# Kernel optimization log

Measured on AMD Instinct MI355X. Metric: run time of the kernel, lower is better.

## Reference

```python
import jax, jax.numpy as jnp
import numpy as np

N = 10000        # nodes
E = 320000       # edges
IN = 256         # input_dim
D = 64           # output_dim per head
H = 4            # num_heads
ED = 32          # edge_dim
T = 8            # num_etypes
SLOPE = 0.2      # leaky relu negative slope


def setup_inputs() -> dict:
    key = jax.random.key(0)
    ks = jax.random.split(key, 12)
    s = 0.05
    feat = jax.random.normal(ks[0], (N, IN), jnp.float32)
    edge_weight = jax.random.uniform(ks[1], (E,), jnp.float32)
    row = jax.random.randint(ks[2], (E,), 0, N, jnp.int32)
    col = jax.random.randint(ks[3], (E,), 0, N, jnp.int32)
    etype_idxs = jax.random.randint(ks[4], (E,), 0, T, jnp.int32)
    W = jax.random.normal(ks[5], (IN, D * H), jnp.float32) * s
    edge_emb_table = jax.random.normal(ks[6], (T, ED), jnp.float32) * s
    W_r = jax.random.normal(ks[7], (T, ED, ED * H), jnp.float32) * s
    a_l = jax.random.normal(ks[8], (H, D), jnp.float32) * s
    a_r = jax.random.normal(ks[9], (H, D), jnp.float32) * s
    a_e = jax.random.normal(ks[10], (H, ED), jnp.float32) * s
    W_res = jax.random.normal(ks[11], (IN, D * H), jnp.float32) * s
    b_res = jnp.zeros((D * H,), jnp.float32)
    return dict(feat=feat, edge_weight=edge_weight, row=row, col=col,
                etype_idxs=etype_idxs, W=W, edge_emb_table=edge_emb_table,
                W_r=W_r, a_l=a_l, a_r=a_r, a_e=a_e, W_res=W_res, b_res=b_res)


def reference(feat, edge_weight, row, col, etype_idxs, W, edge_emb_table,
              W_r, a_l, a_r, a_e, W_res, b_res):
    # node projection: [N, H, D]
    emb = jnp.nan_to_num(feat @ W).reshape(N, H, D)
    # typed linear on edge-type embeddings: only T distinct outputs, gather per edge
    type_out = jnp.einsum('ti,tio->to', edge_emb_table, W_r).reshape(T, H, ED)
    edge_e = type_out[etype_idxs]                      # [E, H, ED]
    # attention logits
    hl = jnp.einsum('nhd,hd->nh', emb, a_l)            # [N, H]
    hr = jnp.einsum('nhd,hd->nh', emb, a_r)            # [N, H]
    he = jnp.einsum('ehd,hd->eh', edge_e, a_e)         # [E, H]
    att = jax.nn.sigmoid(jax.nn.leaky_relu(hl[row] + hr[col] + he, SLOPE))
    att = att * edge_weight[:, None]                   # [E, H]
    # u_mul_e + sum scatter: src=row, dst=col
    msg = emb[row] * att[:, :, None]                   # [E, H, D]
    agg = jax.ops.segment_sum(msg, col, num_segments=N)  # [N, H, D]
    # original permutes to [N, D, H] before flattening
    out = jnp.transpose(agg, (0, 2, 1)).reshape(N, D * H)
    out = out + feat @ W_res + b_res                   # residual
    return jax.nn.elu(out)
```

## Files before the change

### kernel.cpp

```cpp
#include <hip/hip_runtime.h>
#include <hip/hip_bf16.h>
#include <math.h>

#define N_NODES 10000
#define MPAD 10112
#define N_EDGES 320000
#define IN_DIM 256
#define NH 4
#define EDIM 32
#define NT 8
#define SLOPE 0.2f
#define CAP 96

#define WTW (512 * 256)
#define GB (MPAD / 64)
#define EBT 512
#define EB ((N_EDGES + EBT - 1) / EBT)

typedef __attribute__((ext_vector_type(8))) short short8b;
typedef __attribute__((ext_vector_type(4))) float f32x4;

__device__ __forceinline__ float bf2f(ushort u) {
  return __uint_as_float(((unsigned)u) << 16);
}
__device__ __forceinline__ ushort f2bf(float f) {
  __hip_bfloat16 h = __float2bfloat16(f);
  return *(ushort*)&h;
}
__device__ __forceinline__ unsigned pk2(float a, float b) {
  return (unsigned)f2bf(a) | ((unsigned)f2bf(b) << 16);
}

__global__ void prep_kernel(const float* __restrict__ W,
                            const float* __restrict__ W_res,
                            const float* __restrict__ table,
                            const float* __restrict__ W_r,
                            const float* __restrict__ a_e,
                            ushort* __restrict__ Wtb,
                            float* __restrict__ he_type,
                            int* __restrict__ cnt) {
  int i = blockIdx.x * 256 + threadIdx.x;
  if (i < WTW) {
    int c = i >> 8, k = i & 255;
    float v = (c < 256) ? W[k * 256 + ((c & 3) * 64 + (c >> 2))]
                        : W_res[k * 256 + (c - 256)];
    Wtb[c * 256 + k] = f2bf(v);
  } else if (i < WTW + 1024) {
    int t2 = i - WTW;
    int t = t2 >> 7, h = (t2 >> 5) & 3, d = t2 & 31;
    float acc = 0.f;
    for (int q = 0; q < EDIM; ++q)
      acc += table[t * EDIM + q] * W_r[(t * EDIM + q) * (EDIM * NH) + h * EDIM + d];
    acc *= a_e[h * EDIM + d];
#pragma unroll
    for (int o = 16; o; o >>= 1) acc += __shfl_xor(acc, o, 32);
    if (d == 0) he_type[t * NH + h] = acc;
  } else {
    int z = i - WTW - 1024;
    if (z <= N_NODES) cnt[z] = 0;
  }
}

__global__ __launch_bounds__(512) void gemm_bucket_kernel(
    const float* __restrict__ feat, const ushort* __restrict__ Wtb,
    const float* __restrict__ b_res,
    const float* __restrict__ a_l, const float* __restrict__ a_r,
    ushort* __restrict__ emb_t, ushort* __restrict__ resb,
    float* __restrict__ hl, float* __restrict__ hr,
    const int* __restrict__ row, const int* __restrict__ colv,
    const int* __restrict__ et, const float* __restrict__ ew,
    int* cnt, uint2* __restrict__ slots) {
  __shared__ ushort As[64 * 256];
  const int tid = threadIdx.x;

  if (blockIdx.x >= GB) {
    int e = (blockIdx.x - GB) * EBT + tid;
    if (e < N_EDGES) {
      int r = row[e], c = colv[e], t = et[e];
      float w = ew[e];
      uint2 slot;
      slot.x = ((unsigned)t << 16) | (unsigned)r;
      slot.y = __float_as_uint(w);
      int s = atomicAdd(&cnt[c], 1);
      if (s < CAP) slots[(size_t)c * CAP + s] = slot;
    }
    return;
  }

  const int rowbase = blockIdx.x * 64;

#pragma unroll
  for (int i = 0; i < 4; ++i) {
    int c = tid + i * 512;
    int rowl = c >> 5, slot = c & 31;
    int gr = rowbase + rowl;
    uint4 pk = make_uint4(0, 0, 0, 0);
    if (gr < N_NODES) {
      float4 x = *(const float4*)&feat[(size_t)gr * 256 + slot * 8];
      float4 y = *(const float4*)&feat[(size_t)gr * 256 + slot * 8 + 4];
      pk.x = pk2(x.x, x.y); pk.y = pk2(x.z, x.w);
      pk.z = pk2(y.x, y.y); pk.w = pk2(y.z, y.w);
    }
    int idx = rowl * 256 + (((slot * 16) ^ ((rowl & 7) << 4)) >> 1);
    *(uint4*)&As[idx] = pk;
  }
  __syncthreads();

  const int wave = tid >> 6, lane = tid & 63;
  const int col0 = wave * 64;
  const int lr = lane & 15;
  const int lkq = lane >> 4;
  f32x4 acc[4][4] = {};
  const ushort* Bb = Wtb + (size_t)(col0 + lr) * 256 + lkq * 8;

#pragma unroll
  for (int ks = 0; ks < 8; ++ks) {
    short8b a[4], b[4];
#pragma unroll
    for (int m = 0; m < 4; ++m) {
      int rowl = m * 16 + lr;
      int kb = ks * 64 + lkq * 16;
      int idx = rowl * 256 + ((kb ^ ((rowl & 7) << 4)) >> 1);
      a[m] = *(const short8b*)&As[idx];
    }
#pragma unroll
    for (int n = 0; n < 4; ++n)
      b[n] = *(const short8b*)(Bb + (size_t)(n * 16) * 256 + ks * 32);
#pragma unroll
    for (int n = 0; n < 4; ++n)
#pragma unroll
      for (int m = 0; m < 4; ++m)
        acc[n][m] = __builtin_amdgcn_mfma_f32_16x16x32_bf16(b[n], a[m], acc[n][m], 0, 0, 0);
  }

  float pl[4][4] = {{0.f}}, pr[4][4] = {{0.f}};
  if (col0 < 256) {
#pragma unroll
    for (int m = 0; m < 4; ++m) {
      int r = rowbase + m * 16 + lr;
      if (r < N_NODES) {
#pragma unroll
        for (int n = 0; n < 4; ++n) {
          int d = (col0 >> 2) + n * 4 + lkq;
          ushort4 pk4;
          pk4.x = f2bf(acc[n][m][0]); pk4.y = f2bf(acc[n][m][1]);
          pk4.z = f2bf(acc[n][m][2]); pk4.w = f2bf(acc[n][m][3]);
          *(ushort4*)&emb_t[((size_t)r * 64 + d) * 4] = pk4;
        }
      }
    }
#pragma unroll
    for (int n = 0; n < 4; ++n) {
      int d = (col0 >> 2) + n * 4 + lkq;
#pragma unroll
      for (int h = 0; h < 4; ++h) {
        float alv = a_l[h * 64 + d];
        float arv = a_r[h * 64 + d];
#pragma unroll
        for (int m = 0; m < 4; ++m) {
          pl[m][h] = fmaf(acc[n][m][h], alv, pl[m][h]);
          pr[m][h] = fmaf(acc[n][m][h], arv, pr[m][h]);
        }
      }
    }
#pragma unroll
    for (int m = 0; m < 4; ++m)
#pragma unroll
      for (int h = 0; h < 4; ++h) {
        pl[m][h] += __shfl_xor(pl[m][h], 16);
        pl[m][h] += __shfl_xor(pl[m][h], 32);
        pr[m][h] += __shfl_xor(pr[m][h], 16);
        pr[m][h] += __shfl_xor(pr[m][h], 32);
      }
  } else {
#pragma unroll
    for (int m = 0; m < 4; ++m) {
      int r = rowbase + m * 16 + lr;
      if (r < N_NODES) {
#pragma unroll
        for (int n = 0; n < 4; ++n) {
          int c = (col0 - 256) + n * 16 + lkq * 4;
          float4 br = *(const float4*)&b_res[c];
          ushort4 pk4;
          pk4.x = f2bf(acc[n][m][0] + br.x); pk4.y = f2bf(acc[n][m][1] + br.y);
          pk4.z = f2bf(acc[n][m][2] + br.z); pk4.w = f2bf(acc[n][m][3] + br.w);
          *(ushort4*)&resb[(size_t)r * 256 + c] = pk4;
        }
      }
    }
  }

  float* PL = (float*)As;
  float* PR = PL + 1024;
  __syncthreads();
  if (col0 < 256 && lkq == 0) {
#pragma unroll
    for (int m = 0; m < 4; ++m)
#pragma unroll
      for (int h = 0; h < 4; ++h) {
        PL[(wave * 64 + m * 16 + lr) * 4 + h] = pl[m][h];
        PR[(wave * 64 + m * 16 + lr) * 4 + h] = pr[m][h];
      }
  }
  __syncthreads();
  if (tid < 128) {
    int rl = tid >> 1, sel = tid & 1;
    const float* P = sel ? PR : PL;
    float4 v;
    v.x = P[rl * 4 + 0] + P[256 + rl * 4 + 0] + P[512 + rl * 4 + 0] + P[768 + rl * 4 + 0];
    v.y = P[rl * 4 + 1] + P[256 + rl * 4 + 1] + P[512 + rl * 4 + 1] + P[768 + rl * 4 + 1];
    v.z = P[rl * 4 + 2] + P[256 + rl * 4 + 2] + P[512 + rl * 4 + 2] + P[768 + rl * 4 + 2];
    v.w = P[rl * 4 + 3] + P[256 + rl * 4 + 3] + P[512 + rl * 4 + 3] + P[768 + rl * 4 + 3];
    int gr = rowbase + rl;
    if (gr < N_NODES) *(float4*)&(sel ? hr : hl)[gr * 4] = v;
  }
}

__global__ __launch_bounds__(256) void agg_kernel(
    const int* __restrict__ cnt, const uint2* __restrict__ slots,
    const float* __restrict__ hl, const float* __restrict__ hr,
    const float* __restrict__ he_type,
    const ushort* __restrict__ emb_t, const ushort* __restrict__ resb,
    float* __restrict__ out) {
  __shared__ uint4 meta[4 * CAP];
  const int wv = threadIdx.x >> 6;
  const int lane = threadIdx.x & 63;
  const int nu = __builtin_amdgcn_readfirstlane(blockIdx.x * 4 + wv);
  const int cn = min(cnt[nu], CAP);

  {
    float4 R = *(const float4*)&hr[nu * 4];
    for (int j = lane; j < cn; j += 64) {
      uint2 s = slots[(size_t)nu * CAP + j];
      int src = s.x & 0xffff, t = s.x >> 16;
      float w = __uint_as_float(s.y);
      float4 L = *(const float4*)&hl[src * 4];
      float4 He = *(const float4*)&he_type[t * 4];
      float x[4] = {L.x + R.x + He.x, L.y + R.y + He.y,
                    L.z + R.z + He.z, L.w + R.w + He.w};
      float a[4];
#pragma unroll
      for (int h = 0; h < 4; ++h) {
        float v = x[h];
        v = v >= 0.f ? v : SLOPE * v;
        a[h] = w / (1.f + __expf(-v));
      }
      uint4 m;
      m.x = pk2(a[0], a[1]);
      m.y = pk2(a[2], a[3]);
      m.z = (unsigned)src;
      m.w = 0;
      meta[wv * CAP + j] = m;
    }
  }
  __syncthreads();

  float acc0 = 0.f, acc1 = 0.f, acc2 = 0.f, acc3 = 0.f;
  const uint4* mb = &meta[wv * CAP];

#define AGG_FMA(V, WA, WB)                                      \
  acc0 = fmaf(bf2f((V).x), __uint_as_float((WA) << 16), acc0);  \
  acc1 = fmaf(bf2f((V).y), __uint_as_float((WA) & 0xffff0000u), acc1); \
  acc2 = fmaf(bf2f((V).z), __uint_as_float((WB) << 16), acc2);  \
  acc3 = fmaf(bf2f((V).w), __uint_as_float((WB) & 0xffff0000u), acc3);

  const int j4 = cn & ~3;
#pragma unroll 2
  for (int j = 0; j < j4; j += 4) {
    uint4 m0 = mb[j], m1 = mb[j + 1], m2 = mb[j + 2], m3 = mb[j + 3];
    ushort4 v0 = *(const ushort4*)&emb_t[((size_t)m0.z * 64 + lane) * 4];
    ushort4 v1 = *(const ushort4*)&emb_t[((size_t)m1.z * 64 + lane) * 4];
    ushort4 v2 = *(const ushort4*)&emb_t[((size_t)m2.z * 64 + lane) * 4];
    ushort4 v3 = *(const ushort4*)&emb_t[((size_t)m3.z * 64 + lane) * 4];
    AGG_FMA(v0, m0.x, m0.y)
    AGG_FMA(v1, m1.x, m1.y)
    AGG_FMA(v2, m2.x, m2.y)
    AGG_FMA(v3, m3.x, m3.y)
  }
  for (int j = j4; j < cn; ++j) {
    uint4 m0 = mb[j];
    ushort4 v0 = *(const ushort4*)&emb_t[((size_t)m0.z * 64 + lane) * 4];
    AGG_FMA(v0, m0.x, m0.y)
  }
#undef AGG_FMA

  ushort4 r4 = *(const ushort4*)&resb[((size_t)nu * 64 + lane) * 4];
  float v0 = acc0 + bf2f(r4.x), v1 = acc1 + bf2f(r4.y);
  float v2 = acc2 + bf2f(r4.z), v3 = acc3 + bf2f(r4.w);
  float4 o;
  o.x = v0 > 0.f ? v0 : expm1f(v0);
  o.y = v1 > 0.f ? v1 : expm1f(v1);
  o.z = v2 > 0.f ? v2 : expm1f(v2);
  o.w = v3 > 0.f ? v3 : expm1f(v3);
  *(float4*)&out[((size_t)nu * 64 + lane) * 4] = o;
}

extern "C" void kernel_launch(void* const* d_in, const int* in_sizes, int n_in,
                              void* d_out, int out_size, void* d_ws, size_t ws_size,
                              hipStream_t stream) {
  const float* feat = (const float*)d_in[0];
  const float* ew = (const float*)d_in[1];
  const int* row = (const int*)d_in[2];
  const int* col = (const int*)d_in[3];
  const int* etype = (const int*)d_in[4];
  const float* W = (const float*)d_in[5];
  const float* table = (const float*)d_in[6];
  const float* W_r = (const float*)d_in[7];
  const float* a_l = (const float*)d_in[8];
  const float* a_r = (const float*)d_in[9];
  const float* a_e = (const float*)d_in[10];
  const float* W_res = (const float*)d_in[11];
  const float* b_res = (const float*)d_in[12];
  float* out = (float*)d_out;

  char* w = (char*)d_ws;
  auto alloc = [&](size_t bytes) {
    char* pp = w;
    w += (bytes + 255) & ~(size_t)255;
    return pp;
  };
  ushort* Wtb = (ushort*)alloc((size_t)512 * 256 * 2);
  ushort* emb_t = (ushort*)alloc((size_t)N_NODES * 256 * 2);
  ushort* resb = (ushort*)alloc((size_t)N_NODES * 256 * 2);
  uint2* slots = (uint2*)alloc((size_t)N_NODES * CAP * 8);
  float* hl = (float*)alloc((size_t)N_NODES * NH * 4);
  float* hr = (float*)alloc((size_t)N_NODES * NH * 4);
  float* he_type = (float*)alloc(NT * NH * 4);
  int* cnt = (int*)alloc((size_t)(N_NODES + 1) * 4);

  const int PREP_BLOCKS = WTW / 256 + 4 + (N_NODES + 256) / 256;
  prep_kernel<<<PREP_BLOCKS, 256, 0, stream>>>(W, W_res, table, W_r, a_e,
                                               Wtb, he_type, cnt);
  gemm_bucket_kernel<<<GB + EB, 512, 0, stream>>>(
      feat, Wtb, b_res, a_l, a_r, emb_t, resb, hl, hr,
      row, col, etype, ew, cnt, slots);
  agg_kernel<<<N_NODES / 4, 256, 0, stream>>>(cnt, slots, hl, hr, he_type,
                                              emb_t, resb, out);
}
```

Before: 52.38 us.

## Split node embeddings into two feature planes and aggregate each plane separately

```diff
diff --git a/kernel.cpp b/kernel.cpp
--- a/kernel.cpp
+++ b/kernel.cpp
@@ -65,7 +65,8 @@
     const float* __restrict__ feat, const ushort* __restrict__ Wtb,
     const float* __restrict__ b_res,
     const float* __restrict__ a_l, const float* __restrict__ a_r,
-    ushort* __restrict__ emb_t, ushort* __restrict__ resb,
+    ushort* __restrict__ embA, ushort* __restrict__ embB,
+    ushort* __restrict__ resb,
     float* __restrict__ hl, float* __restrict__ hr,
     const int* __restrict__ row, const int* __restrict__ colv,
     const int* __restrict__ et, const float* __restrict__ ew,
@@ -135,6 +136,7 @@
 
   float pl[4][4] = {{0.f}}, pr[4][4] = {{0.f}};
   if (col0 < 256) {
+    ushort* plane = (col0 >= 128) ? embB : embA;
 #pragma unroll
     for (int m = 0; m < 4; ++m) {
       int r = rowbase + m * 16 + lr;
@@ -142,10 +144,11 @@
 #pragma unroll
         for (int n = 0; n < 4; ++n) {
           int d = (col0 >> 2) + n * 4 + lkq;
+          int dp = d & 31;
           ushort4 pk4;
           pk4.x = f2bf(acc[n][m][0]); pk4.y = f2bf(acc[n][m][1]);
           pk4.z = f2bf(acc[n][m][2]); pk4.w = f2bf(acc[n][m][3]);
-          *(ushort4*)&emb_t[((size_t)r * 64 + d) * 4] = pk4;
+          *(ushort4*)&plane[((size_t)r * 32 + dp) * 4] = pk4;
         }
       }
     }
@@ -220,13 +223,16 @@
     const int* __restrict__ cnt, const uint2* __restrict__ slots,
     const float* __restrict__ hl, const float* __restrict__ hr,
     const float* __restrict__ he_type,
-    const ushort* __restrict__ emb_t, const ushort* __restrict__ resb,
-    float* __restrict__ out) {
+    const ushort* __restrict__ embA, const ushort* __restrict__ embB,
+    const ushort* __restrict__ resb, float* __restrict__ out) {
   __shared__ uint4 meta[4 * CAP];
+  const int P = blockIdx.y;
+  const ushort* emb_p = P ? embB : embA;
   const int wv = threadIdx.x >> 6;
   const int lane = threadIdx.x & 63;
   const int nu = __builtin_amdgcn_readfirstlane(blockIdx.x * 4 + wv);
   const int cn = min(cnt[nu], CAP);
+  const int cn4 = (cn + 3) & ~3;
 
   {
     float4 R = *(const float4*)&hr[nu * 4];
@@ -252,11 +258,15 @@
       m.w = 0;
       meta[wv * CAP + j] = m;
     }
+    for (int j = cn + lane; j < cn4; j += 64)
+      meta[wv * CAP + j] = make_uint4(0, 0, 0, 0);
   }
   __syncthreads();
 
   float acc0 = 0.f, acc1 = 0.f, acc2 = 0.f, acc3 = 0.f;
   const uint4* mb = &meta[wv * CAP];
+  const int eh = lane >> 5;
+  const int dp = lane & 31;
 
 #define AGG_FMA(V, WA, WB)                                      \
   acc0 = fmaf(bf2f((V).x), __uint_as_float((WA) << 16), acc0);  \
@@ -264,35 +274,34 @@
   acc2 = fmaf(bf2f((V).z), __uint_as_float((WB) << 16), acc2);  \
   acc3 = fmaf(bf2f((V).w), __uint_as_float((WB) & 0xffff0000u), acc3);
 
-  const int j4 = cn & ~3;
 #pragma unroll 2
-  for (int j = 0; j < j4; j += 4) {
-    uint4 m0 = mb[j], m1 = mb[j + 1], m2 = mb[j + 2], m3 = mb[j + 3];
-    ushort4 v0 = *(const ushort4*)&emb_t[((size_t)m0.z * 64 + lane) * 4];
-    ushort4 v1 = *(const ushort4*)&emb_t[((size_t)m1.z * 64 + lane) * 4];
-    ushort4 v2 = *(const ushort4*)&emb_t[((size_t)m2.z * 64 + lane) * 4];
-    ushort4 v3 = *(const ushort4*)&emb_t[((size_t)m3.z * 64 + lane) * 4];
+  for (int j = 0; j < cn4; j += 4) {
+    uint4 m0 = mb[j + eh];
+    uint4 m1 = mb[j + 2 + eh];
+    ushort4 v0 = *(const ushort4*)&emb_p[((size_t)m0.z * 32 + dp) * 4];
+    ushort4 v1 = *(const ushort4*)&emb_p[((size_t)m1.z * 32 + dp) * 4];
     AGG_FMA(v0, m0.x, m0.y)
     AGG_FMA(v1, m1.x, m1.y)
-    AGG_FMA(v2, m2.x, m2.y)
-    AGG_FMA(v3, m3.x, m3.y)
-  }
-  for (int j = j4; j < cn; ++j) {
-    uint4 m0 = mb[j];
-    ushort4 v0 = *(const ushort4*)&emb_t[((size_t)m0.z * 64 + lane) * 4];
-    AGG_FMA(v0, m0.x, m0.y)
   }
 #undef AGG_FMA
 
-  ushort4 r4 = *(const ushort4*)&resb[((size_t)nu * 64 + lane) * 4];
-  float v0 = acc0 + bf2f(r4.x), v1 = acc1 + bf2f(r4.y);
-  float v2 = acc2 + bf2f(r4.z), v3 = acc3 + bf2f(r4.w);
-  float4 o;
-  o.x = v0 > 0.f ? v0 : expm1f(v0);
-  o.y = v1 > 0.f ? v1 : expm1f(v1);
-  o.z = v2 > 0.f ? v2 : expm1f(v2);
-  o.w = v3 > 0.f ? v3 : expm1f(v3);
-  *(float4*)&out[((size_t)nu * 64 + lane) * 4] = o;
+  acc0 += __shfl_xor(acc0, 32);
+  acc1 += __shfl_xor(acc1, 32);
+  acc2 += __shfl_xor(acc2, 32);
+  acc3 += __shfl_xor(acc3, 32);
+
+  if (lane < 32) {
+    int dg = P * 32 + lane;
+    ushort4 r4 = *(const ushort4*)&resb[((size_t)nu * 64 + dg) * 4];
+    float v0 = acc0 + bf2f(r4.x), v1 = acc1 + bf2f(r4.y);
+    float v2 = acc2 + bf2f(r4.z), v3 = acc3 + bf2f(r4.w);
+    float4 o;
+    o.x = v0 > 0.f ? v0 : expm1f(v0);
+    o.y = v1 > 0.f ? v1 : expm1f(v1);
+    o.z = v2 > 0.f ? v2 : expm1f(v2);
+    o.w = v3 > 0.f ? v3 : expm1f(v3);
+    *(float4*)&out[((size_t)nu * 64 + dg) * 4] = o;
+  }
 }
 
 extern "C" void kernel_launch(void* const* d_in, const int* in_sizes, int n_in,
@@ -320,7 +329,8 @@
     return pp;
   };
   ushort* Wtb = (ushort*)alloc((size_t)512 * 256 * 2);
-  ushort* emb_t = (ushort*)alloc((size_t)N_NODES * 256 * 2);
+  ushort* embA = (ushort*)alloc((size_t)N_NODES * 128 * 2);
+  ushort* embB = (ushort*)alloc((size_t)N_NODES * 128 * 2);
   ushort* resb = (ushort*)alloc((size_t)N_NODES * 256 * 2);
   uint2* slots = (uint2*)alloc((size_t)N_NODES * CAP * 8);
   float* hl = (float*)alloc((size_t)N_NODES * NH * 4);
@@ -332,8 +342,8 @@
   prep_kernel<<<PREP_BLOCKS, 256, 0, stream>>>(W, W_res, table, W_r, a_e,
                                                Wtb, he_type, cnt);
   gemm_bucket_kernel<<<GB + EB, 512, 0, stream>>>(
-      feat, Wtb, b_res, a_l, a_r, emb_t, resb, hl, hr,
+      feat, Wtb, b_res, a_l, a_r, embA, embB, resb, hl, hr,
       row, col, etype, ew, cnt, slots);
-  agg_kernel<<<N_NODES / 4, 256, 0, stream>>>(cnt, slots, hl, hr, he_type,
-                                              emb_t, resb, out);
-}
+  agg_kernel<<<dim3(N_NODES / 4, 2), 256, 0, stream>>>(
+      cnt, slots, hl, hr, he_type, embA, embB, resb, out);
+}
```

Result: slower. 53.91 us (+2.9%).
